# Performance work log

Measured on AMD Instinct MI355X. Metric: run time of the kernel, lower is better.

The kernel has to match this reference:

```python
import jax, jax.numpy as jnp
import numpy as np

N_NODES = 50000
N_EDGES = 800000
D = 64
H = 128


def setup_inputs() -> dict:
    key = jax.random.key(0)
    ks = jax.random.split(key, 6)
    x = jax.random.normal(ks[0], (N_NODES, D), dtype=jnp.float32)
    edge_index = jax.random.randint(ks[1], (2, N_EDGES), 0, N_NODES, dtype=jnp.int64)
    # GIN MLP params (Linear(D->H) -> ReLU -> Linear(H->D))
    W1 = jax.random.normal(ks[2], (D, H), dtype=jnp.float32) * (1.0 / np.sqrt(D))
    b1 = jnp.zeros((H,), dtype=jnp.float32)
    W2 = jax.random.normal(ks[3], (H, D), dtype=jnp.float32) * (1.0 / np.sqrt(H))
    b2 = jnp.zeros((D,), dtype=jnp.float32)
    eps = jnp.zeros((1, 1), dtype=jnp.float32)  # trainable eps parameter
    return {"x": x, "W1": W1, "b1": b1, "W2": W2, "b2": b2, "eps": eps,
            "edge_index": edge_index}


def reference(x, W1, b1, W2, b2, eps, edge_index):
    src, dst = edge_index[0], edge_index[1]
    # node -> edge gather (0th-order ptensor on each edge = sum of endpoint feats)
    msg = x[src] + x[dst]                                    # [E, D]
    # edge -> node gather: each node sums messages of its incident edges
    agg = (jax.ops.segment_sum(msg, src, num_segments=N_NODES)
           + jax.ops.segment_sum(msg, dst, num_segments=N_NODES))  # [N, D]
    ones = jnp.ones((N_EDGES,), dtype=x.dtype)
    deg = (jax.ops.segment_sum(ones, src, num_segments=N_NODES)
           + jax.ops.segment_sum(ones, dst, num_segments=N_NODES))  # [N]
    # subtract deg*x so aggregation reduces to the plain neighbor sum (GIN)
    neighbor = agg - x * deg[:, None]
    out = (1.0 + eps) * x + neighbor                          # eps is [1,1], broadcasts
    # GIN MLP
    h = jax.nn.relu(out @ W1 + b1)
    return h @ W2 + b2
```

## Files before the change

kernel.cpp:

```cpp
#include <hip/hip_runtime.h>


#define D 64
#define H 128
#define MPW 8
#define REGSH 6
#define REGSZ 64
#define P1_BLOCKS 256
#define EVBUF_SZ 6400
#define NR_MAX 1024
#define NCAP 96
#define PSTR 68

typedef __attribute__((ext_vector_type(8))) short short8;
typedef __attribute__((ext_vector_type(4))) float float4v;

__device__ __forceinline__ float lane_bcast(float v, int l) {
    return __uint_as_float(__builtin_amdgcn_readlane(__float_as_uint(v), l));
}

__device__ __forceinline__ unsigned short f2bf(float f) {
    unsigned int u = __float_as_uint(f);
    u = (u + (((u >> 16) & 1u) + 0x7fffu)) >> 16;
    return (unsigned short)u;
}

__device__ __forceinline__ void bf2_acc(unsigned int u, float& a, float& b) {
    a += __uint_as_float(u << 16);
    b += __uint_as_float(u & 0xffff0000u);
}

__global__ void zero_int_kernel(int* __restrict__ p, int n) {
    int i = blockIdx.x * blockDim.x + threadIdx.x;
    if (i < n) p[i] = 0;
}

__global__ void zero_f_kernel(float* __restrict__ p, int n) {
    int i = blockIdx.x * blockDim.x + threadIdx.x;
    if (i < n) p[i] = 0.0f;
}

__global__ void prep_kernel(unsigned int* __restrict__ xh2, int npairs,
                            int* __restrict__ cursor, int NR, int CAPB,
                            const float* __restrict__ W1,
                            const float* __restrict__ W2,
                            unsigned short* __restrict__ wsW1,
                            unsigned short* __restrict__ wsW2) {
    int i = blockIdx.x * blockDim.x + threadIdx.x;
    if (i < NR) cursor[i] = i * CAPB;
    if (i < 32) xh2[npairs + i] = 0;
    if (i < 8192) {
        int j = i & 7, ln = (i >> 3) & 63;
        int q = (ln >> 4) & 3;
        int tt1 = (i >> 9) & 7, s1 = i >> 12;
        wsW1[i] = f2bf(W1[(s1 * 32 + q * 8 + j) * H + tt1 * 16 + (ln & 15)]);
        int tt2 = (i >> 9) & 3, s2 = i >> 11;
        wsW2[i] = f2bf(W2[(s2 * 32 + q * 8 + j) * D + tt2 * 16 + (ln & 15)]);
    }
}

__global__ __launch_bounds__(256) void part1_kernel(
    const int* __restrict__ src, const int* __restrict__ dst,
    int* __restrict__ cursor, unsigned int* __restrict__ evarr,
    const float* __restrict__ x, unsigned int* __restrict__ xh2, int npairs,
    int E, int N, int NR, int CAPB, int EPB)
{
    __shared__ unsigned int evbuf[EVBUF_SZ];
    __shared__ int hist[NR_MAX];
    int t = threadIdx.x;

    int gstride = gridDim.x * 256;
    for (int i = blockIdx.x * 256 + t; i < npairs; i += gstride) {
        float2 v = *(const float2*)(x + (size_t)i * 2);
        unsigned int a = __float_as_uint(v.x);
        unsigned int b = __float_as_uint(v.y);
        a = (a + (((a >> 16) & 1u) + 0x7fffu)) >> 16;
        b = (b + (((b >> 16) & 1u) + 0x7fffu)) >> 16;
        xh2[i] = a | (b << 16);
    }

    for (int b = t; b < NR; b += 256) hist[b] = 0;
    __syncthreads();

    int e0 = blockIdx.x * EPB;
    int ne = E - e0; if (ne > EPB) ne = EPB; if (ne < 0) ne = 0;
    for (int i = t; i < ne; i += 256) {
        int s = src[e0 + i], d = dst[e0 + i];
        s = (s < 0) ? 0 : ((s >= N) ? N - 1 : s);
        d = (d < 0) ? 0 : ((d >= N) ? N - 1 : d);
        evbuf[2 * i]     = ((unsigned int)s << 16) | (unsigned int)d;
        evbuf[2 * i + 1] = ((unsigned int)d << 16) | (unsigned int)s;
        atomicAdd(&hist[s >> REGSH], 1);
        atomicAdd(&hist[d >> REGSH], 1);
    }
    __syncthreads();

    for (int b = t; b < NR; b += 256) {
        int c = hist[b];
        hist[b] = c ? atomicAdd(&cursor[b], c) : 0;
    }
    __syncthreads();

    int nev = 2 * ne;
    for (int i = t; i < nev; i += 256) {
        unsigned int ev = evbuf[i];
        int b = (int)(ev >> (16 + REGSH));
        int slot = atomicAdd(&hist[b], 1);
        if (slot < (b + 1) * CAPB) evarr[slot] = ev;
    }
}

__global__ __launch_bounds__(512) void part2_fused(
    const unsigned int* __restrict__ evarr, const int* __restrict__ cursor,
    const unsigned short* __restrict__ xh, const float* __restrict__ x,
    const float* __restrict__ epsp,
    const unsigned short* __restrict__ wsW1,
    const unsigned short* __restrict__ wsW2,
    const float* __restrict__ b1, const float* __restrict__ b2,
    float* __restrict__ y, int N, int CAPB)
{
    __shared__ unsigned short nbuf[REGSZ * NCAP + 32];
    __shared__ int scnt[REGSZ];
    __shared__ float pre_lds[REGSZ * PSTR];
    __shared__ unsigned short sW1[8192];
    __shared__ unsigned short sW2[8192];
    __shared__ unsigned short hbuf[4 * 16 * H];
    int t = threadIdx.x;
    int b = blockIdx.x;
    if (t < REGSZ) scnt[t] = 0;
#pragma unroll
    for (int i = 0; i < 2; ++i) {
        ((uint4*)sW1)[t + i * 512] = ((const uint4*)wsW1)[t + i * 512];
        ((uint4*)sW2)[t + i * 512] = ((const uint4*)wsW2)[t + i * 512];
    }
    __syncthreads();

    int base = b * CAPB;
    int count = cursor[b] - base;
    if (count < 0) count = 0;
    if (count > CAPB) count = CAPB;

    for (int i = t; i < count; i += 512) {
        unsigned int ev = evarr[base + i];
        int row = (int)((ev >> 16) & (REGSZ - 1));
        int k = atomicAdd(&scnt[row], 1);
        if (k < NCAP) nbuf[row * NCAP + k] = (unsigned short)(ev & 0xffffu);
    }
    __syncthreads();

    int wave = t >> 6, lane = t & 63;
    int r = lane >> 5;
    int h = lane & 31;
    float e1 = 1.0f + epsp[0];

    for (int k = 0; k < 8; ++k) {
        int n = wave * 8 + k;
        int v = b * REGSZ + n;
        int m = (v < N) ? scnt[n] : 0;
        m = (m > NCAP) ? NCAP : m;
        float f0 = 0.0f, f1 = 0.0f;
        for (int j = 0; j < m; j += 32) {
            int cc[16];
#pragma unroll
            for (int q = 0; q < 16; ++q) {
                int ii = j + 2 * q + r;
                int c = (int)nbuf[n * NCAP + ii];
                cc[q] = (ii < m) ? c : N;
            }
            unsigned int u[16];
#pragma unroll
            for (int q = 0; q < 16; ++q)
                u[q] = *(const unsigned int*)(xh + (size_t)cc[q] * D + 2 * h);
#pragma unroll
            for (int q = 0; q < 16; ++q) bf2_acc(u[q], f0, f1);
        }
        f0 += __shfl_xor(f0, 32, 64);
        f1 += __shfl_xor(f1, 32, 64);
        if (r == 0) {
            float2 sv = make_float2(0.0f, 0.0f);
            if (v < N) sv = *(const float2*)(x + (size_t)v * D + 2 * h);
            pre_lds[n * PSTR + 2 * h]     = f0 + e1 * sv.x;
            pre_lds[n * PSTR + 2 * h + 1] = f1 + e1 * sv.y;
        }
    }
    __syncthreads();

    int p = wave >> 1, hh = wave & 1;
    int quad = lane >> 4, lm = lane & 15;
    int row0 = p * 16 + lm;

    short8 a1[2];
#pragma unroll
    for (int s = 0; s < 2; ++s) {
        const float* rp = &pre_lds[row0 * PSTR + s * 32 + quad * 8];
        float4v p0 = *(const float4v*)rp;
        float4v p1 = *(const float4v*)(rp + 4);
        short8 a;
        a[0] = (short)f2bf(p0[0]); a[1] = (short)f2bf(p0[1]);
        a[2] = (short)f2bf(p0[2]); a[3] = (short)f2bf(p0[3]);
        a[4] = (short)f2bf(p1[0]); a[5] = (short)f2bf(p1[1]);
        a[6] = (short)f2bf(p1[2]); a[7] = (short)f2bf(p1[3]);
        a1[s] = a;
    }

    float4v acc1[4];
#pragma unroll
    for (int i = 0; i < 4; ++i) {
        int tt = hh * 4 + i;
        float bb = b1[tt * 16 + lm];
        float4v c = {bb, bb, bb, bb};
#pragma unroll
        for (int s = 0; s < 2; ++s) {
            short8 bw = *(const short8*)&sW1[((s * 8 + tt) * 64 + lane) * 8];
            c = __builtin_amdgcn_mfma_f32_16x16x32_bf16(a1[s], bw, c, 0, 0, 0);
        }
        acc1[i] = c;
    }

    unsigned short* hb = &hbuf[p * 16 * H];
#pragma unroll
    for (int i = 0; i < 4; ++i) {
        int tt = hh * 4 + i;
#pragma unroll
        for (int rr = 0; rr < 4; ++rr) {
            float hv = fmaxf(acc1[i][rr], 0.0f);
            hb[(quad * 4 + rr) * H + tt * 16 + lm] = f2bf(hv);
        }
    }
    __syncthreads();

    short8 a2[4];
#pragma unroll
    for (int s = 0; s < 4; ++s)
        a2[s] = *(const short8*)&hb[lm * H + s * 32 + quad * 8];

    int v0t = b * REGSZ + p * 16;
#pragma unroll
    for (int i = 0; i < 2; ++i) {
        int tt = hh * 2 + i;
        float bb = b2[tt * 16 + lm];
        float4v c = {bb, bb, bb, bb};
#pragma unroll
        for (int s = 0; s < 4; ++s) {
            short8 bw = *(const short8*)&sW2[((s * 4 + tt) * 64 + lane) * 8];
            c = __builtin_amdgcn_mfma_f32_16x16x32_bf16(a2[s], bw, c, 0, 0, 0);
        }
#pragma unroll
        for (int rr = 0; rr < 4; ++rr) {
            int v = v0t + quad * 4 + rr;
            if (v < N) y[(size_t)v * D + tt * 16 + lm] = c[rr];
        }
    }
}


__global__ void count_kernel(const int* __restrict__ ei, int* __restrict__ deg,
                             int twoE, int N) {
    int i = blockIdx.x * blockDim.x + threadIdx.x;
    if (i < twoE) {
        int v = ei[i];
        v = (v < 0) ? 0 : ((v >= N) ? N - 1 : v);
        atomicAdd(&deg[v], 1);
    }
}

__global__ __launch_bounds__(256) void scan_part1(const int* __restrict__ deg,
                                                  int* __restrict__ bsum, int n) {
    __shared__ int red[256];
    int t = threadIdx.x;
    int i = blockIdx.x * 256 + t;
    red[t] = (i < n) ? deg[i] : 0;
    __syncthreads();
    for (int off = 128; off > 0; off >>= 1) {
        if (t < off) red[t] += red[t + off];
        __syncthreads();
    }
    if (t == 0) bsum[blockIdx.x] = red[0];
}

__global__ __launch_bounds__(256) void scan_part2(const int* __restrict__ bsum,
                                                  int* __restrict__ boff,
                                                  int* __restrict__ rowstart_n, int nb) {
    __shared__ int s[256];
    int t = threadIdx.x;
    int v = (t < nb) ? bsum[t] : 0;
    s[t] = v;
    __syncthreads();
    for (int off = 1; off < 256; off <<= 1) {
        int u = (t >= off) ? s[t - off] : 0;
        __syncthreads();
        s[t] += u;
        __syncthreads();
    }
    if (t < nb) boff[t] = s[t] - v;
    if (t == 255) *rowstart_n = s[255];
}

__global__ __launch_bounds__(256) void scan_part3(const int* __restrict__ deg,
                                                  const int* __restrict__ boff,
                                                  int* __restrict__ rowstart,
                                                  int* __restrict__ cursor, int n) {
    __shared__ int s[256];
    int t = threadIdx.x;
    int i = blockIdx.x * 256 + t;
    int v = (i < n) ? deg[i] : 0;
    s[t] = v;
    __syncthreads();
    for (int off = 1; off < 256; off <<= 1) {
        int u = (t >= off) ? s[t - off] : 0;
        __syncthreads();
        s[t] += u;
        __syncthreads();
    }
    if (i < n) {
        int r = boff[blockIdx.x] + s[t] - v;
        rowstart[i] = r;
        cursor[i] = r;
    }
}

__global__ __launch_bounds__(256) void scan_single(const int* __restrict__ deg,
                                                   int* __restrict__ rowstart,
                                                   int* __restrict__ cursor,
                                                   int n, int chunk) {
    __shared__ int psum[256];
    int t = threadIdx.x;
    int lo = t * chunk;
    int hi = lo + chunk; if (hi > n) hi = n;
    int s = 0;
    for (int i = lo; i < hi; ++i) s += deg[i];
    psum[t] = s;
    __syncthreads();
    for (int off = 1; off < 256; off <<= 1) {
        int v = (t >= off) ? psum[t - off] : 0;
        __syncthreads();
        psum[t] += v;
        __syncthreads();
    }
    int run = (t == 0) ? 0 : psum[t - 1];
    for (int i = lo; i < hi; ++i) {
        int d = deg[i];
        rowstart[i] = run;
        cursor[i] = run;
        run += d;
    }
    if (t == 255) rowstart[n] = psum[255];
}

__global__ __launch_bounds__(256) void fill_xcd(
    const int* __restrict__ src, const int* __restrict__ dst,
    int* __restrict__ cursor, int* __restrict__ col,
    int E, int N, int npg)
{
    int grp = blockIdx.x & 7;
    int slice = blockIdx.x >> 3;
    int lo = grp * npg;
    int hi = lo + npg; if (hi > N) hi = N;
    int stride = (gridDim.x >> 3) * 256;
    for (int i = slice * 256 + threadIdx.x; i < E; i += stride) {
        int s = src[i], d = dst[i];
        s = (s < 0) ? 0 : ((s >= N) ? N - 1 : s);
        d = (d < 0) ? 0 : ((d >= N) ? N - 1 : d);
        if (s >= lo && s < hi) { int p = atomicAdd(&cursor[s], 1); col[p] = d; }
        if (d >= lo && d < hi) { int q = atomicAdd(&cursor[d], 1); col[q] = s; }
    }
}

__global__ __launch_bounds__(256) void gather_csr2(
    const float* __restrict__ x, const float* __restrict__ epsp,
    const int* __restrict__ rowstart, const int* __restrict__ col,
    float* __restrict__ pre, int N)
{
    int wid = (blockIdx.x * 256 + threadIdx.x) >> 6;
    int lane = threadIdx.x & 63;
    int v0 = wid * 2;
    if (v0 >= N) return;
    int v1 = v0 + 1;
    float eps1 = 1.0f + epsp[0];
    int j0 = rowstart[v0], re0 = rowstart[v0 + 1];
    float a0 = eps1 * x[(size_t)v0 * D + lane];
    int j1 = 0, re1 = 0;
    float a1 = 0.0f;
    if (v1 < N) {
        j1 = rowstart[v1]; re1 = rowstart[v1 + 1];
        a1 = eps1 * x[(size_t)v1 * D + lane];
    }
    while (j0 + 8 <= re0 && j1 + 8 <= re1) {
        float p0 = x[(size_t)col[j0 + 0] * D + lane];
        float p1 = x[(size_t)col[j0 + 1] * D + lane];
        float p2 = x[(size_t)col[j0 + 2] * D + lane];
        float p3 = x[(size_t)col[j0 + 3] * D + lane];
        float p4 = x[(size_t)col[j0 + 4] * D + lane];
        float p5 = x[(size_t)col[j0 + 5] * D + lane];
        float p6 = x[(size_t)col[j0 + 6] * D + lane];
        float p7 = x[(size_t)col[j0 + 7] * D + lane];
        float q0 = x[(size_t)col[j1 + 0] * D + lane];
        float q1 = x[(size_t)col[j1 + 1] * D + lane];
        float q2 = x[(size_t)col[j1 + 2] * D + lane];
        float q3 = x[(size_t)col[j1 + 3] * D + lane];
        float q4 = x[(size_t)col[j1 + 4] * D + lane];
        float q5 = x[(size_t)col[j1 + 5] * D + lane];
        float q6 = x[(size_t)col[j1 + 6] * D + lane];
        float q7 = x[(size_t)col[j1 + 7] * D + lane];
        a0 += ((p0 + p1) + (p2 + p3)) + ((p4 + p5) + (p6 + p7));
        a1 += ((q0 + q1) + (q2 + q3)) + ((q4 + q5) + (q6 + q7));
        j0 += 8; j1 += 8;
    }
    for (; j0 + 8 <= re0; j0 += 8) {
        float p0 = x[(size_t)col[j0 + 0] * D + lane];
        float p1 = x[(size_t)col[j0 + 1] * D + lane];
        float p2 = x[(size_t)col[j0 + 2] * D + lane];
        float p3 = x[(size_t)col[j0 + 3] * D + lane];
        float p4 = x[(size_t)col[j0 + 4] * D + lane];
        float p5 = x[(size_t)col[j0 + 5] * D + lane];
        float p6 = x[(size_t)col[j0 + 6] * D + lane];
        float p7 = x[(size_t)col[j0 + 7] * D + lane];
        a0 += ((p0 + p1) + (p2 + p3)) + ((p4 + p5) + (p6 + p7));
    }
    for (; j1 + 8 <= re1; j1 += 8) {
        float q0 = x[(size_t)col[j1 + 0] * D + lane];
        float q1 = x[(size_t)col[j1 + 1] * D + lane];
        float q2 = x[(size_t)col[j1 + 2] * D + lane];
        float q3 = x[(size_t)col[j1 + 3] * D + lane];
        float q4 = x[(size_t)col[j1 + 4] * D + lane];
        float q5 = x[(size_t)col[j1 + 5] * D + lane];
        float q6 = x[(size_t)col[j1 + 6] * D + lane];
        float q7 = x[(size_t)col[j1 + 7] * D + lane];
        a1 += ((q0 + q1) + (q2 + q3)) + ((q4 + q5) + (q6 + q7));
    }
    for (; j0 < re0; ++j0) a0 += x[(size_t)col[j0] * D + lane];
    for (; j1 < re1; ++j1) a1 += x[(size_t)col[j1] * D + lane];
    pre[(size_t)v0 * D + lane] = a0;
    if (v1 < N) pre[(size_t)v1 * D + lane] = a1;
}

__device__ __forceinline__ void mlp_store(
    const float* acc, float* sW, int v0, int t, int lane, int nNodes,
    const float* __restrict__ W2,
    const float* __restrict__ b1, const float* __restrict__ b2,
    float* __restrict__ y)
{
    float b1a = b1[lane], b1b = b1[lane + 64];
    float ha[MPW], hb[MPW];
#pragma unroll
    for (int m = 0; m < MPW; ++m) { ha[m] = b1a; hb[m] = b1b; }
#pragma unroll 4
    for (int f = 0; f < D; ++f) {
        float wa = sW[f * H + lane];
        float wb = sW[f * H + lane + 64];
#pragma unroll
        for (int m = 0; m < MPW; ++m) {
            float o = lane_bcast(acc[m], f);
            ha[m] += o * wa;
            hb[m] += o * wb;
        }
    }
#pragma unroll
    for (int m = 0; m < MPW; ++m) {
        ha[m] = fmaxf(ha[m], 0.0f);
        hb[m] = fmaxf(hb[m], 0.0f);
    }

    __syncthreads();
    for (int i = t; i < H * D; i += 256) sW[i] = W2[i];
    __syncthreads();

    float b2v = b2[lane];
    float yv[MPW];
#pragma unroll
    for (int m = 0; m < MPW; ++m) yv[m] = b2v;
#pragma unroll 4
    for (int k = 0; k < 64; ++k) {
        float w = sW[k * D + lane];
#pragma unroll
        for (int m = 0; m < MPW; ++m) yv[m] += lane_bcast(ha[m], k) * w;
    }
#pragma unroll 4
    for (int k = 0; k < 64; ++k) {
        float w = sW[(k + 64) * D + lane];
#pragma unroll
        for (int m = 0; m < MPW; ++m) yv[m] += lane_bcast(hb[m], k) * w;
    }
#pragma unroll
    for (int m = 0; m < MPW; ++m) {
        int v = v0 + m;
        if (v < nNodes) y[(size_t)v * D + lane] = yv[m];
    }
}

__global__ __launch_bounds__(256) void mlp_pre(
    const float* __restrict__ pre, const float* __restrict__ W1,
    const float* __restrict__ b1, const float* __restrict__ W2,
    const float* __restrict__ b2, float* __restrict__ y, int nNodes)
{
    __shared__ float sW[D * H];
    int t = threadIdx.x;
    for (int i = t; i < D * H; i += 256) sW[i] = W1[i];
    __syncthreads();
    int wave = t >> 6, lane = t & 63;
    int v0 = (blockIdx.x * 4 + wave) * MPW;
    float acc[MPW];
#pragma unroll
    for (int m = 0; m < MPW; ++m) {
        int v = v0 + m;
        acc[m] = (v < nNodes) ? pre[(size_t)v * D + lane] : 0.0f;
    }
    mlp_store(acc, sW, v0, t, lane, nNodes, W2, b1, b2, y);
}

__global__ __launch_bounds__(256) void gather_mlp_csr(
    const float* __restrict__ x, const float* __restrict__ W1,
    const float* __restrict__ b1, const float* __restrict__ W2,
    const float* __restrict__ b2, const float* __restrict__ epsp,
    const int* __restrict__ rowstart, const int* __restrict__ col,
    float* __restrict__ y, int nNodes)
{
    __shared__ float sW[D * H];
    int t = threadIdx.x;
    for (int i = t; i < D * H; i += 256) sW[i] = W1[i];
    __syncthreads();
    int wave = t >> 6, lane = t & 63;
    float eps1 = 1.0f + epsp[0];
    int v0 = (blockIdx.x * 4 + wave) * MPW;
    float acc[MPW];
#pragma unroll
    for (int m = 0; m < MPW; ++m) {
        int v = v0 + m;
        float a = 0.0f;
        if (v < nNodes) {
            int rs = rowstart[v], re = rowstart[v + 1];
            a = eps1 * x[(size_t)v * D + lane];
            int j = rs;
            for (; j + 8 <= re; j += 8) {
                float p0 = x[(size_t)col[j + 0] * D + lane];
                float p1 = x[(size_t)col[j + 1] * D + lane];
                float p2 = x[(size_t)col[j + 2] * D + lane];
                float p3 = x[(size_t)col[j + 3] * D + lane];
                float p4 = x[(size_t)col[j + 4] * D + lane];
                float p5 = x[(size_t)col[j + 5] * D + lane];
                float p6 = x[(size_t)col[j + 6] * D + lane];
                float p7 = x[(size_t)col[j + 7] * D + lane];
                a += ((p0 + p1) + (p2 + p3)) + ((p4 + p5) + (p6 + p7));
            }
            for (; j < re; ++j) a += x[(size_t)col[j] * D + lane];
        }
        acc[m] = a;
    }
    mlp_store(acc, sW, v0, t, lane, nNodes, W2, b1, b2, y);
}

__global__ void scatter_kernel(const float* __restrict__ x,
                               const int* __restrict__ src,
                               const int* __restrict__ dst,
                               float* __restrict__ agg, int E, int N)
{
    int tid = blockIdx.x * blockDim.x + threadIdx.x;
    int e = tid >> 6, lane = tid & 63;
    if (e < E) {
        int s = src[e], d = dst[e];
        s = (s < 0) ? 0 : ((s >= N) ? N - 1 : s);
        d = (d < 0) ? 0 : ((d >= N) ? N - 1 : d);
        float xs = x[(size_t)s * D + lane];
        float xd = x[(size_t)d * D + lane];
        atomicAdd(&agg[(size_t)s * D + lane], xd);
        atomicAdd(&agg[(size_t)d * D + lane], xs);
    }
}

__global__ __launch_bounds__(256) void mlp_from_agg(
    const float* __restrict__ x, const float* __restrict__ W1,
    const float* __restrict__ b1, const float* __restrict__ W2,
    const float* __restrict__ b2, const float* __restrict__ epsp,
    float* __restrict__ yio, int nNodes)
{
    __shared__ float sW[D * H];
    int t = threadIdx.x;
    for (int i = t; i < D * H; i += 256) sW[i] = W1[i];
    __syncthreads();
    int wave = t >> 6, lane = t & 63;
    float eps1 = 1.0f + epsp[0];
    int v0 = (blockIdx.x * 4 + wave) * MPW;
    float acc[MPW];
#pragma unroll
    for (int m = 0; m < MPW; ++m) {
        int v = v0 + m;
        acc[m] = (v < nNodes)
                   ? (eps1 * x[(size_t)v * D + lane] + yio[(size_t)v * D + lane])
                   : 0.0f;
    }
    mlp_store(acc, sW, v0, t, lane, nNodes, W2, b1, b2, yio);
}

extern "C" void kernel_launch(void* const* d_in, const int* in_sizes, int n_in,
                              void* d_out, int out_size, void* d_ws, size_t ws_size,
                              hipStream_t stream)
{
    const float* x   = (const float*)d_in[0];
    const float* W1  = (const float*)d_in[1];
    const float* b1  = (const float*)d_in[2];
    const float* W2  = (const float*)d_in[3];
    const float* b2  = (const float*)d_in[4];
    const float* eps = (const float*)d_in[5];
    const int*   ei  = (const int*)d_in[6];
    float* out = (float*)d_out;

    int N = in_sizes[0] / D;
    int E = in_sizes[6] / 2;
    const int* src = ei;
    const int* dst = ei + E;

    int nb = (N + 255) / 256;

    int NR = (N + REGSZ - 1) >> REGSH;
    int meanE = (NR > 0) ? (2 * E + NR - 1) / NR : 0;
    int CAPB = meanE + meanE / 4 + 128;
    int EPB = (E + P1_BLOCKS - 1) / P1_BLOCKS;
    size_t off_cur  = 0;
    size_t off_ev   = (off_cur + (size_t)NR * 4 + 15) & ~(size_t)15;
    size_t off_xh   = (off_ev + (size_t)NR * CAPB * 4 + 15) & ~(size_t)15;
    size_t off_w1   = (off_xh + (size_t)(N + 1) * D * 2 + 15) & ~(size_t)15;
    size_t off_w2   = off_w1 + 8192 * 2;
    size_t need_part = off_w2 + 8192 * 2;

    size_t csr_ints = (size_t)(3 * N + 1 + 2 * E) + 512;
    size_t need_csr = csr_ints * sizeof(int);
    size_t need_split = need_csr + (size_t)N * D * sizeof(float);
    int mlp_blocks = (N + 4 * MPW - 1) / (4 * MPW);

    if (ws_size >= need_part && N >= REGSZ && N <= 65535
        && NR <= NR_MAX && 2 * EPB <= EVBUF_SZ && (N * D) % 2 == 0) {
        char* base = (char*)d_ws;
        int*            cursor = (int*)(base + off_cur);
        unsigned int*   evarr  = (unsigned int*)(base + off_ev);
        unsigned short* xh     = (unsigned short*)(base + off_xh);
        unsigned short* wsW1   = (unsigned short*)(base + off_w1);
        unsigned short* wsW2   = (unsigned short*)(base + off_w2);
        int npairs = N * D / 2;

        prep_kernel<<<32, 256, 0, stream>>>(
            (unsigned int*)xh, npairs, cursor, NR, CAPB, W1, W2, wsW1, wsW2);
        part1_kernel<<<P1_BLOCKS, 256, 0, stream>>>(
            src, dst, cursor, evarr, x, (unsigned int*)xh, npairs,
            E, N, NR, CAPB, EPB);
        part2_fused<<<NR, 512, 0, stream>>>(
            evarr, cursor, xh, x, eps, wsW1, wsW2, b1, b2, out, N, CAPB);
    } else if (ws_size >= need_csr) {
        int*   deg      = (int*)d_ws;
        int*   cursor   = deg + N;
        int*   rowstart = cursor + N;
        int*   col      = rowstart + (N + 1);
        int*   bsum     = col + 2 * E;
        int*   boff     = bsum + 256;
        float* pre      = (float*)(boff + 256);

        zero_int_kernel<<<(N + 255) / 256, 256, 0, stream>>>(deg, N);
        count_kernel<<<(2 * E + 255) / 256, 256, 0, stream>>>(ei, deg, 2 * E, N);
        if (nb <= 256) {
            scan_part1<<<nb, 256, 0, stream>>>(deg, bsum, N);
            scan_part2<<<1, 256, 0, stream>>>(bsum, boff, &rowstart[N], nb);
            scan_part3<<<nb, 256, 0, stream>>>(deg, boff, rowstart, cursor, N);
        } else {
            int chunk = (N + 255) / 256;
            scan_single<<<1, 256, 0, stream>>>(deg, rowstart, cursor, N, chunk);
        }
        fill_xcd<<<2048, 256, 0, stream>>>(src, dst, cursor, col, E, N, (N + 7) / 8);
        int waves = (N + 1) / 2;
        int gather_blocks = (waves + 3) / 4;
        if (ws_size >= need_split) {
            gather_csr2<<<gather_blocks, 256, 0, stream>>>(x, eps, rowstart, col, pre, N);
            mlp_pre<<<mlp_blocks, 256, 0, stream>>>(pre, W1, b1, W2, b2, out, N);
        } else {
            gather_mlp_csr<<<mlp_blocks, 256, 0, stream>>>(
                x, W1, b1, W2, b2, eps, rowstart, col, out, N);
        }
    } else {
        int nd = N * D;
        zero_f_kernel<<<(nd + 255) / 256, 256, 0, stream>>>(out, nd);
        long long st = (long long)E * 64;
        scatter_kernel<<<(int)((st + 255) / 256), 256, 0, stream>>>(x, src, dst, out, E, N);
        mlp_from_agg<<<mlp_blocks, 256, 0, stream>>>(x, W1, b1, W2, b2, eps, out, N);
    }
}
```

Baseline: 150.0 us.

## Locally sort edge events by region before scattering to global buckets

The binning kernel now records each event's ticket from the histogram atomics, runs a block-wide prefix scan to get local region offsets, and counting-sorts events into shared memory. Global writes then go out in region order, so consecutive threads write contiguous addresses and the second round of shared atomics is gone. This costs extra shared memory (a sort buffer and a ticket buffer), which may lower occupancy, plus a scan with several barriers.

```diff
diff --git a/kernel.cpp b/kernel.cpp
--- a/kernel.cpp
+++ b/kernel.cpp
@@ -66,7 +66,12 @@
     int E, int N, int NR, int CAPB, int EPB)
 {
     __shared__ unsigned int evbuf[EVBUF_SZ];
+    __shared__ unsigned int sortbuf[EVBUF_SZ];
+    __shared__ unsigned short tickbuf[EVBUF_SZ];
     __shared__ int hist[NR_MAX];
+    __shared__ int lbase[NR_MAX];
+    __shared__ int gbase[NR_MAX];
+    __shared__ int scanw[256];
     int t = threadIdx.x;
 
     int gstride = gridDim.x * 256;
@@ -88,25 +93,56 @@
         int s = src[e0 + i], d = dst[e0 + i];
         s = (s < 0) ? 0 : ((s >= N) ? N - 1 : s);
         d = (d < 0) ? 0 : ((d >= N) ? N - 1 : d);
-        evbuf[2 * i]     = ((unsigned int)s << 16) | (unsigned int)d;
-        evbuf[2 * i + 1] = ((unsigned int)d << 16) | (unsigned int)s;
-        atomicAdd(&hist[s >> REGSH], 1);
-        atomicAdd(&hist[d >> REGSH], 1);
-    }
-    __syncthreads();
+        unsigned int ev0 = ((unsigned int)s << 16) | (unsigned int)d;
+        unsigned int ev1 = ((unsigned int)d << 16) | (unsigned int)s;
+        int k0 = atomicAdd(&hist[s >> REGSH], 1);
+        int k1 = atomicAdd(&hist[d >> REGSH], 1);
+        evbuf[2 * i]     = ev0; tickbuf[2 * i]     = (unsigned short)k0;
+        evbuf[2 * i + 1] = ev1; tickbuf[2 * i + 1] = (unsigned short)k1;
+    }
+    __syncthreads();
+
+    {
+        int i0 = t * 4;
+        int h0 = (i0 + 0 < NR) ? hist[i0 + 0] : 0;
+        int h1 = (i0 + 1 < NR) ? hist[i0 + 1] : 0;
+        int h2 = (i0 + 2 < NR) ? hist[i0 + 2] : 0;
+        int h3 = (i0 + 3 < NR) ? hist[i0 + 3] : 0;
+        int s4 = h0 + h1 + h2 + h3;
+        scanw[t] = s4;
+        __syncthreads();
+        for (int off = 1; off < 256; off <<= 1) {
+            int u = (t >= off) ? scanw[t - off] : 0;
+            __syncthreads();
+            scanw[t] += u;
+            __syncthreads();
+        }
+        int run = scanw[t] - s4;
+        if (i0 + 0 < NR) { lbase[i0 + 0] = run; run += h0; }
+        if (i0 + 1 < NR) { lbase[i0 + 1] = run; run += h1; }
+        if (i0 + 2 < NR) { lbase[i0 + 2] = run; run += h2; }
+        if (i0 + 3 < NR) { lbase[i0 + 3] = run; run += h3; }
+    }
 
     for (int b = t; b < NR; b += 256) {
         int c = hist[b];
-        hist[b] = c ? atomicAdd(&cursor[b], c) : 0;
+        gbase[b] = c ? atomicAdd(&cursor[b], c) : 0;
     }
     __syncthreads();
 
     int nev = 2 * ne;
     for (int i = t; i < nev; i += 256) {
         unsigned int ev = evbuf[i];
-        int b = (int)(ev >> (16 + REGSH));
-        int slot = atomicAdd(&hist[b], 1);
-        if (slot < (b + 1) * CAPB) evarr[slot] = ev;
+        int reg = (int)(ev >> (16 + REGSH));
+        sortbuf[lbase[reg] + (int)tickbuf[i]] = ev;
+    }
+    __syncthreads();
+
+    for (int i = t; i < nev; i += 256) {
+        unsigned int ev = sortbuf[i];
+        int reg = (int)(ev >> (16 + REGSH));
+        int addr = gbase[reg] + (i - lbase[reg]);
+        if (addr < (reg + 1) * CAPB) evarr[addr] = ev;
     }
 }
 
```

New measurement: 146.8 us. -2.1%, faster.
